# Performance work log

Hardware: AMD Instinct MI355X
Metric: run time of the kernel (lower is better)

Reference implementation:

```python
import jax, jax.numpy as jnp
from jax import lax
import numpy as np

B, T, D, L = 128, 512, 300, 25
H = D // 2  # per-direction LSTM hidden (input_dim // 2)


def setup_inputs() -> dict:
    key = jax.random.key(0)
    ks = jax.random.split(key, 16)
    s = 0.1
    def n(k, shape):
        return jax.random.normal(k, shape, dtype=jnp.float32) * s
    lengths = jax.random.randint(ks[0], (B,), T // 4, T + 1)
    mask = (jnp.arange(T)[None, :] < lengths[:, None]).astype(jnp.float32)
    labels = jax.random.randint(ks[1], (B, T), 0, L)
    return {
        "input_embed": jax.random.normal(ks[2], (B, T, D), dtype=jnp.float32),
        "mask": mask,
        "labels": labels,
        "Wih_f": n(ks[3], (4 * H, D)), "Whh_f": n(ks[4], (4 * H, H)),
        "bih_f": n(ks[5], (4 * H,)), "bhh_f": n(ks[6], (4 * H,)),
        "Wih_b": n(ks[7], (4 * H, D)), "Whh_b": n(ks[8], (4 * H, H)),
        "bih_b": n(ks[9], (4 * H,)), "bhh_b": n(ks[10], (4 * H,)),
        "Wl": n(ks[11], (L, D)), "bl": n(ks[12], (L,)),
        "trans": n(ks[13], (L, L)),
        "start_trans": n(ks[14], (L,)),
        "end_trans": n(ks[15], (L,)),
    }


def _lstm(x, Wih, Whh, bih, bhh):
    # x: (B, T, D) -> hidden states (B, T, H); PyTorch gate order i,f,g,o
    b = bih + bhh
    h0 = jnp.zeros((x.shape[0], H), x.dtype)
    c0 = jnp.zeros((x.shape[0], H), x.dtype)
    def step(carry, xt):
        h, c = carry
        g = xt @ Wih.T + h @ Whh.T + b
        i, f, gg, o = jnp.split(g, 4, axis=-1)
        c = jax.nn.sigmoid(f) * c + jax.nn.sigmoid(i) * jnp.tanh(gg)
        h = jax.nn.sigmoid(o) * jnp.tanh(c)
        return (h, c), h
    _, hs = lax.scan(step, (h0, c0), jnp.swapaxes(x, 0, 1))
    return jnp.swapaxes(hs, 0, 1)


def _emissions(input_embed, mask, Wih_f, Whh_f, bih_f, bhh_f, Wih_b, Whh_b, bih_b, bhh_b, Wl, bl):
    lengths = mask.sum(1).astype(jnp.int32)  # (B,)
    h_f = _lstm(input_embed, Wih_f, Whh_f, bih_f, bhh_f)
    # per-sequence reversal (pack_padded_sequence semantics for the bwd dir)
    idx = jnp.clip(lengths[:, None] - 1 - jnp.arange(T)[None, :], 0, T - 1)  # (B, T)
    idx3 = jnp.broadcast_to(idx[:, :, None], input_embed.shape)
    x_rev = jnp.take_along_axis(input_embed, idx3, axis=1)
    h_b_rev = _lstm(x_rev, Wih_b, Whh_b, bih_b, bhh_b)
    h_b = jnp.take_along_axis(h_b_rev, jnp.broadcast_to(idx[:, :, None], h_b_rev.shape), axis=1)
    # pad_packed_sequence zeros padded positions
    h = jnp.concatenate([h_f, h_b], axis=-1) * mask[:, :, None]
    out = (h @ Wl.T + bl) * mask[:, :, None]  # out *= mask.unsqueeze(-1)
    return out


def _crf_numerator(out, labels, mask, trans, start_trans, end_trans):
    lengths = mask.sum(1).astype(jnp.int32)
    emit = jnp.take_along_axis(out, labels[:, :, None], axis=2)[..., 0]  # (B, T)
    emit_score = jnp.sum(emit * mask, axis=1)
    trans_score = jnp.sum(trans[labels[:, :-1], labels[:, 1:]] * mask[:, 1:], axis=1)
    ar = jnp.arange(out.shape[0])
    y_last = labels[ar, lengths - 1]
    return start_trans[labels[:, 0]] + emit_score + trans_score + end_trans[y_last]


def _crf_denominator(out, mask, trans, start_trans, end_trans):
    alpha0 = start_trans[None, :] + out[:, 0]  # (B, L)
    e_seq = jnp.swapaxes(out, 0, 1)[1:]  # (T-1, B, L)
    m_seq = mask.T[1:]  # (T-1, B)
    def step(alpha, inp):
        e_t, m_t = inp
        new = jax.nn.logsumexp(alpha[:, :, None] + trans[None, :, :], axis=1) + e_t
        alpha = jnp.where((m_t > 0)[:, None], new, alpha)
        return alpha, None
    alpha, _ = lax.scan(step, alpha0, (e_seq, m_seq))
    return jax.nn.logsumexp(alpha + end_trans[None, :], axis=1)


def _viterbi(out, mask, trans, start_trans, end_trans):
    delta0 = start_trans[None, :] + out[:, 0]
    e_seq = jnp.swapaxes(out, 0, 1)[1:]
    m_seq = mask.T[1:]
    ident = jnp.arange(L, dtype=jnp.int32)[None, :]
    def step(delta, inp):
        e_t, m_t = inp
        s = delta[:, :, None] + trans[None, :, :]  # (B, L_prev, L_cur)
        bp = jnp.argmax(s, axis=1).astype(jnp.int32)
        new = jnp.max(s, axis=1) + e_t
        v = (m_t > 0)[:, None]
        return jnp.where(v, new, delta), jnp.where(v, bp, ident)
    delta, bps = lax.scan(step, delta0, (e_seq, m_seq))
    last = jnp.argmax(delta + end_trans[None, :], axis=1).astype(jnp.int32)  # (B,)
    def back(lab, bp):
        prev = jnp.take_along_axis(bp, lab[:, None], axis=1)[:, 0]
        return prev, lab
    lab0, rest = lax.scan(back, last, bps, reverse=True)  # rest[k] = label at t=k+1
    path = jnp.concatenate([lab0[None, :], rest], axis=0)  # (T, B)
    return path.T  # (B, T); positions past each length repeat trailing labels (masked anyway)


def reference(input_embed, mask, labels, Wih_f, Whh_f, bih_f, bhh_f, Wih_b, Whh_b, bih_b, bhh_b, Wl, bl, trans, start_trans, end_trans):
    out = _emissions(input_embed, mask, Wih_f, Whh_f, bih_f, bhh_f, Wih_b, Whh_b, bih_b, bhh_b, Wl, bl)
    score = _crf_numerator(out, labels, mask, trans, start_trans, end_trans) - _crf_denominator(out, mask, trans, start_trans, end_trans)
    loss = -jnp.mean(score)
    path = _viterbi(out, mask, trans, start_trans, end_trans)
    return loss, path
```

## Files before the change

kernel.cpp:

```cpp
#include <hip/hip_runtime.h>
#include <math.h>

#define Bn 128
#define Tn 512
#define Dn 300
#define Hn 150
#define Gn 600
#define Ln 25

__global__ __launch_bounds__(64) void k_len(const float* __restrict__ mask, int* __restrict__ lens) {
  int b = blockIdx.x, lane = threadIdx.x;
  float s = 0.f;
  for (int t = lane; t < Tn; t += 64) s += mask[b * Tn + t];
#pragma unroll
  for (int off = 32; off; off >>= 1) s += __shfl_xor(s, off);
  if (lane == 0) lens[b] = (int)(s + 0.5f);
}

__global__ __launch_bounds__(256) void k_gemm_in(
    const float* __restrict__ X, const float* __restrict__ Wf, const float* __restrict__ Wb,
    const float* __restrict__ bihf, const float* __restrict__ bhhf,
    const float* __restrict__ bihb, const float* __restrict__ bhhb,
    const int* __restrict__ lens, float* __restrict__ XgfC, float* __restrict__ YbC,
    int lo_f, int lo_b, int tshift, int chSh) {
  const int tileR = blockIdx.x;
  const int b = tileR >> tshift;
  const int tloc = (tileR & ((1 << tshift) - 1)) << 6;
  const int dir = (blockIdx.y >= 10);
  const int t_lo = dir ? lo_b : lo_f;
  const int t0g = t_lo + tloc;
  if (t0g >= lens[b]) return;
  const int c0 = (blockIdx.y - dir * 10) << 6;

  __shared__ __align__(16) float As[16][64];
  __shared__ __align__(16) float Bs[16][64];
  const int tid = threadIdx.x;
  const int lr = tid >> 2;
  const int kg = (tid & 3) << 2;
  const int tx = tid & 15, ty = tid >> 4;
  float acc[4][4];
#pragma unroll
  for (int i = 0; i < 4; ++i)
#pragma unroll
    for (int j = 0; j < 4; ++j) acc[i][j] = 0.f;

  const float* Xrow = X + ((size_t)(b * Tn + t0g + lr)) * Dn;
  const int cgl = c0 + lr;
  const float* Wrow = (cgl < Gn) ? ((dir ? Wb : Wf) + (size_t)cgl * Dn) : nullptr;

  for (int k0 = 0; k0 < Dn; k0 += 16) {
    float4 av = make_float4(0.f, 0.f, 0.f, 0.f), bv = make_float4(0.f, 0.f, 0.f, 0.f);
    int k = k0 + kg;
    if (k < Dn) {
      av = *(const float4*)(Xrow + k);
      if (Wrow) bv = *(const float4*)(Wrow + k);
    }
    __syncthreads();
    As[kg + 0][lr] = av.x; As[kg + 1][lr] = av.y; As[kg + 2][lr] = av.z; As[kg + 3][lr] = av.w;
    Bs[kg + 0][lr] = bv.x; Bs[kg + 1][lr] = bv.y; Bs[kg + 2][lr] = bv.z; Bs[kg + 3][lr] = bv.w;
    __syncthreads();
#pragma unroll
    for (int kk = 0; kk < 16; ++kk) {
      float4 a = *(const float4*)(&As[kk][ty << 2]);
      float4 q = *(const float4*)(&Bs[kk][tx << 2]);
      acc[0][0] = fmaf(a.x, q.x, acc[0][0]); acc[0][1] = fmaf(a.x, q.y, acc[0][1]);
      acc[0][2] = fmaf(a.x, q.z, acc[0][2]); acc[0][3] = fmaf(a.x, q.w, acc[0][3]);
      acc[1][0] = fmaf(a.y, q.x, acc[1][0]); acc[1][1] = fmaf(a.y, q.y, acc[1][1]);
      acc[1][2] = fmaf(a.y, q.z, acc[1][2]); acc[1][3] = fmaf(a.y, q.w, acc[1][3]);
      acc[2][0] = fmaf(a.z, q.x, acc[2][0]); acc[2][1] = fmaf(a.z, q.y, acc[2][1]);
      acc[2][2] = fmaf(a.z, q.z, acc[2][2]); acc[2][3] = fmaf(a.z, q.w, acc[2][3]);
      acc[3][0] = fmaf(a.w, q.x, acc[3][0]); acc[3][1] = fmaf(a.w, q.y, acc[3][1]);
      acc[3][2] = fmaf(a.w, q.z, acc[3][2]); acc[3][3] = fmaf(a.w, q.w, acc[3][3]);
    }
  }
  const int cg0 = c0 + (tx << 2);
  if (cg0 >= Gn) return;
  const float* bih = dir ? bihb : bihf;
  const float* bhh = dir ? bhhb : bhhf;
  float* out = dir ? YbC : XgfC;
  const size_t rowbase = ((size_t)b << chSh) + tloc;
#pragma unroll
  for (int i = 0; i < 4; ++i) {
    float4 r;
    r.x = acc[i][0] + bih[cg0 + 0] + bhh[cg0 + 0];
    r.y = acc[i][1] + bih[cg0 + 1] + bhh[cg0 + 1];
    r.z = acc[i][2] + bih[cg0 + 2] + bhh[cg0 + 2];
    r.w = acc[i][3] + bih[cg0 + 3] + bhh[cg0 + 3];
    *(float4*)(out + (rowbase + (ty << 2) + i) * Gn + cg0) = r;
  }
}

__global__ __launch_bounds__(640) void k_lstm(
    const float* __restrict__ XgfC, const float* __restrict__ YbC,
    const float* __restrict__ Whf, const float* __restrict__ Whb,
    const int* __restrict__ lens, float* __restrict__ hf, float* __restrict__ hb,
    float* __restrict__ sHf, float* __restrict__ sCf,
    float* __restrict__ sHb, float* __restrict__ sCb,
    int lo_f, int lo_b, int chSh, int CH) {
  __shared__ __align__(16) float h_s[152];
  __shared__ __align__(16) float g_s[Gn];
  const int tid = threadIdx.x;
  const int dir = blockIdx.x >> 7;
  const int b = blockIdx.x & 127;
  const int len = lens[b];
  const int lo = dir ? lo_b : lo_f;
  if (lo >= len) return;
  const int hi = min(lo + CH, len);
  const float* Xg = dir ? YbC : XgfC;
  const float* W = dir ? Whb : Whf;
  float* ho = dir ? hb : hf;
  float* sH = dir ? sHb : sHf;
  float* sC = dir ? sCb : sCf;
  const bool init = dir ? (hi == len) : (lo == 0);

  if (tid < 152) h_s[tid] = 0.f;
  float c = 0.f;
  if (!init && tid < Hn) { h_s[tid] = sH[b * Hn + tid]; c = sC[b * Hn + tid]; }

  const int col = tid;
  float wreg[152];
  if (col < Gn) {
    const float2* wr = (const float2*)(W + (size_t)col * Hn);
#pragma unroll
    for (int k = 0; k < 75; ++k) {
      float2 w2 = wr[k];
      wreg[2 * k] = w2.x; wreg[2 * k + 1] = w2.y;
    }
    wreg[150] = 0.f; wreg[151] = 0.f;
  } else {
#pragma unroll
    for (int k = 0; k < 152; ++k) wreg[k] = 0.f;
  }
  __syncthreads();

  const int nst = hi - lo;
  const size_t cb = ((size_t)b << chSh);
  const size_t bT = (size_t)b * Tn;
  float xcur = 0.f;
  if (col < Gn) xcur = Xg[(cb + (dir ? (hi - 1 - lo) : 0)) * Gn + col];
  for (int s = 0; s < nst; ++s) {
    const int rl = dir ? (hi - 1 - lo - s) : s;
    const int rg = lo + rl;
    float xn = 0.f;
    if (col < Gn && s + 1 < nst) {
      int rln = dir ? (rl - 1) : (rl + 1);
      xn = Xg[(cb + rln) * Gn + col];
    }
    if (col < Gn) {
      float acc = xcur;
#pragma unroll
      for (int q = 0; q < 38; ++q) {
        float4 h4 = *(const float4*)(h_s + (q << 2));
        acc = fmaf(wreg[q * 4 + 0], h4.x, acc);
        acc = fmaf(wreg[q * 4 + 1], h4.y, acc);
        acc = fmaf(wreg[q * 4 + 2], h4.z, acc);
        acc = fmaf(wreg[q * 4 + 3], h4.w, acc);
      }
      g_s[col] = acc;
    }
    xcur = xn;
    __syncthreads();
    if (tid < Hn) {
      float gi = g_s[tid], gf = g_s[tid + 150], gg = g_s[tid + 300], go = g_s[tid + 450];
      float si = 1.f / (1.f + expf(-gi));
      float sf = 1.f / (1.f + expf(-gf));
      float so = 1.f / (1.f + expf(-go));
      c = sf * c + si * tanhf(gg);
      float h = so * tanhf(c);
      h_s[tid] = h;
      ho[(bT + rg) * Hn + tid] = h;
    }
    __syncthreads();
  }
  if (tid < Hn) { sH[b * Hn + tid] = h_s[tid]; sC[b * Hn + tid] = c; }
}

__global__ __launch_bounds__(256) void k_emis(
    const float* __restrict__ hf, const float* __restrict__ hb,
    const float* __restrict__ Wl, const float* __restrict__ bl,
    const int* __restrict__ lens, float* __restrict__ em) {
  int idx = blockIdx.x * 256 + threadIdx.x;
  int row = idx >> 5;
  int l = idx & 31;
  int b = row >> 9, t = row & 511;
  if (l >= Ln || t >= lens[b]) return;
  const float2* hf2 = (const float2*)(hf + (size_t)row * Hn);
  const float2* hb2 = (const float2*)(hb + (size_t)row * Hn);
  const float2* w0 = (const float2*)(Wl + (size_t)l * Dn);
  const float2* w1 = (const float2*)(Wl + (size_t)l * Dn + Hn);
  float acc = bl[l];
#pragma unroll 5
  for (int q = 0; q < 75; ++q) {
    float2 a = hf2[q], w = w0[q];
    acc = fmaf(a.x, w.x, fmaf(a.y, w.y, acc));
    float2 a2 = hb2[q], w2 = w1[q];
    acc = fmaf(a2.x, w2.x, fmaf(a2.y, w2.y, acc));
  }
  em[(size_t)row * Ln + l] = acc;
}

__global__ __launch_bounds__(64) void k_num(
    const float* __restrict__ em, const int* __restrict__ labels, const int* __restrict__ lens,
    const float* __restrict__ trans, const float* __restrict__ st, const float* __restrict__ et,
    float* __restrict__ num) {
  int b = blockIdx.x, lane = threadIdx.x;
  int len = lens[b];
  float s = 0.f;
  for (int t = lane; t < len; t += 64) {
    int lab = labels[b * Tn + t];
    s += em[((size_t)b * Tn + t) * Ln + lab];
    if (t + 1 < len) s += trans[lab * Ln + labels[b * Tn + t + 1]];
  }
#pragma unroll
  for (int off = 32; off; off >>= 1) s += __shfl_xor(s, off);
  if (lane == 0)
    num[b] = s + st[labels[b * Tn]] + et[labels[b * Tn + len - 1]];
}

__global__ __launch_bounds__(64) void k_den(
    const float* __restrict__ em, const int* __restrict__ lens, const float* __restrict__ trans,
    const float* __restrict__ st, const float* __restrict__ et, float* __restrict__ den) {
  __shared__ float E[Ln * Ln];
  __shared__ float p_s[32];
  int b = blockIdx.x, lane = threadIdx.x;
  for (int u = lane; u < Ln * Ln; u += 64) E[u] = expf(trans[u]);
  int len = lens[b];
  const float* ob = em + (size_t)b * Tn * Ln;
  float alpha = -1e30f;
  if (lane < Ln) alpha = st[lane] + ob[lane];
  __syncthreads();
  for (int t = 1; t < len; ++t) {
    float m = alpha;
#pragma unroll
    for (int off = 32; off; off >>= 1) m = fmaxf(m, __shfl_xor(m, off));
    float p = (lane < Ln) ? expf(alpha - m) : 0.f;
    if (lane < 32) p_s[lane] = p;
    __syncthreads();
    if (lane < Ln) {
      float ssum = 0.f;
#pragma unroll
      for (int i = 0; i < Ln; ++i) ssum = fmaf(p_s[i], E[i * Ln + lane], ssum);
      alpha = m + logf(ssum) + ob[(size_t)t * Ln + lane];
    }
    __syncthreads();
  }
  float v = (lane < Ln) ? alpha + et[lane] : -1e30f;
  float m = v;
#pragma unroll
  for (int off = 32; off; off >>= 1) m = fmaxf(m, __shfl_xor(m, off));
  float ex = (lane < Ln) ? expf(v - m) : 0.f;
#pragma unroll
  for (int off = 32; off; off >>= 1) ex += __shfl_xor(ex, off);
  if (lane == 0) den[b] = m + logf(ex);
}

__global__ __launch_bounds__(64) void k_vit(
    const float* __restrict__ em, const int* __restrict__ lens, const float* __restrict__ trans,
    const float* __restrict__ st, const float* __restrict__ et, float* __restrict__ pathf) {
  __shared__ float Tl[Ln * Ln];
  __shared__ float d_s[Ln];
  __shared__ unsigned char bp[Tn * Ln];
  int b = blockIdx.x, lane = threadIdx.x;
  for (int u = lane; u < Ln * Ln; u += 64) Tl[u] = trans[u];
  int len = lens[b];
  const float* ob = em + (size_t)b * Tn * Ln;
  float delta = (lane < Ln) ? st[lane] + ob[lane] : -1e30f;
  __syncthreads();
  for (int t = 1; t < len; ++t) {
    if (lane < Ln) d_s[lane] = delta;
    __syncthreads();
    if (lane < Ln) {
      float best = -1e30f; int bi = 0;
#pragma unroll
      for (int i = 0; i < Ln; ++i) {
        float v = d_s[i] + Tl[i * Ln + lane];
        if (v > best) { best = v; bi = i; }
      }
      bp[t * Ln + lane] = (unsigned char)bi;
      delta = best + ob[(size_t)t * Ln + lane];
    }
    __syncthreads();
  }
  float v = (lane < Ln) ? delta + et[lane] : -1e30f;
  float m = v;
#pragma unroll
  for (int off = 32; off; off >>= 1) m = fmaxf(m, __shfl_xor(m, off));
  unsigned long long eq = __ballot(v == m);
  int last = __ffsll(eq) - 1;
  if (lane == 0) {
    int cur = last;
    for (int t = len - 1; t >= 1; --t) {
      pathf[b * Tn + t] = (float)cur;
      cur = bp[t * Ln + cur];
    }
    pathf[b * Tn + 0] = (float)cur;
  }
  for (int t = len + lane; t < Tn; t += 64)
    pathf[b * Tn + t] = (float)last;
}

__global__ __launch_bounds__(64) void k_loss(const float* __restrict__ num, const float* __restrict__ den,
                                             float* __restrict__ out0) {
  int lane = threadIdx.x;
  float s = (num[lane] - den[lane]) + (num[lane + 64] - den[lane + 64]);
#pragma unroll
  for (int off = 32; off; off >>= 1) s += __shfl_xor(s, off);
  if (lane == 0) out0[0] = -s / (float)Bn;
}

extern "C" void kernel_launch(void* const* d_in, const int* in_sizes, int n_in,
                              void* d_out, int out_size, void* d_ws, size_t ws_size,
                              hipStream_t stream) {
  const float* X = (const float*)d_in[0];
  const float* mask = (const float*)d_in[1];
  const int* labels = (const int*)d_in[2];
  const float* Wihf = (const float*)d_in[3];
  const float* Whhf = (const float*)d_in[4];
  const float* bihf = (const float*)d_in[5];
  const float* bhhf = (const float*)d_in[6];
  const float* Wihb = (const float*)d_in[7];
  const float* Whhb = (const float*)d_in[8];
  const float* bihb = (const float*)d_in[9];
  const float* bhhb = (const float*)d_in[10];
  const float* Wl = (const float*)d_in[11];
  const float* bl = (const float*)d_in[12];
  const float* trans = (const float*)d_in[13];
  const float* st = (const float*)d_in[14];
  const float* et = (const float*)d_in[15];
  float* outv = (float*)d_out;

  auto planBytes = [](int CH) -> size_t {
    return ((size_t)2 * Bn * CH * Gn + 2 * (size_t)Bn * Tn * Hn + (size_t)Bn * Tn * Ln
            + 4 * (size_t)Bn * Hn + 3 * (size_t)Bn) * 4;
  };
  int CH, chSh, tshift;
  if (ws_size >= planBytes(512)) { CH = 512; chSh = 9; tshift = 3; }
  else                           { CH = 64;  chSh = 6; tshift = 0; }
  const int NC = Tn / CH;

  float* ws = (float*)d_ws;
  size_t off = 0;
  float* XgfC = ws + off; off += (size_t)Bn * CH * Gn;
  float* YbC  = ws + off; off += (size_t)Bn * CH * Gn;
  float* hf   = ws + off; off += (size_t)Bn * Tn * Hn;
  float* hb   = ws + off; off += (size_t)Bn * Tn * Hn;
  float* em   = ws + off; off += (size_t)Bn * Tn * Ln;
  float* sHf  = ws + off; off += (size_t)Bn * Hn;
  float* sCf  = ws + off; off += (size_t)Bn * Hn;
  float* sHb  = ws + off; off += (size_t)Bn * Hn;
  float* sCb  = ws + off; off += (size_t)Bn * Hn;
  float* num  = ws + off; off += Bn;
  float* den  = ws + off; off += Bn;
  int* lens   = (int*)(ws + off); off += Bn;

  k_len<<<Bn, 64, 0, stream>>>(mask, lens);

  for (int i = 0; i < NC; ++i) {
    int lo_f = i * CH;
    int lo_b = (NC - 1 - i) * CH;
    dim3 gg(Bn * (CH >> 6), 20);
    k_gemm_in<<<gg, 256, 0, stream>>>(X, Wihf, Wihb, bihf, bhhf, bihb, bhhb,
                                      lens, XgfC, YbC, lo_f, lo_b, tshift, chSh);
    k_lstm<<<2 * Bn, 640, 0, stream>>>(XgfC, YbC, Whhf, Whhb, lens, hf, hb,
                                       sHf, sCf, sHb, sCb, lo_f, lo_b, chSh, CH);
  }

  k_emis<<<(Bn * Tn * 32) / 256, 256, 0, stream>>>(hf, hb, Wl, bl, lens, em);

  k_num<<<Bn, 64, 0, stream>>>(em, labels, lens, trans, st, et, num);
  k_den<<<Bn, 64, 0, stream>>>(em, lens, trans, st, et, den);
  k_vit<<<Bn, 64, 0, stream>>>(em, lens, trans, st, et, outv + 1);
  k_loss<<<1, 64, 0, stream>>>(num, den, outv);
}
```

Before: 2.572 ms.

## Fuse CRF kernels into one launch, double-buffer input GEMM, add chunk sizes

Merges the numerator, forward-algorithm and Viterbi kernels into a single 384-block launch in which each block takes one role. The denominator and Viterbi roles stage emissions in shared memory and hold a transition column in registers, using wave shuffles in place of per-step shared-memory exchanges and barriers. The input-projection GEMM gains a double-buffered shared tile with the next global load issued before compute, dropping one barrier per k-step. Intermediate chunk sizes are added for mid-sized workspaces. The costs are higher register and shared-memory use (about 64KB per CRF block) and possibly lower occupancy.

After: 2.136 ms. -17.0%, faster.

```diff
diff --git a/kernel.cpp b/kernel.cpp
--- a/kernel.cpp
+++ b/kernel.cpp
@@ -32,8 +32,8 @@
   if (t0g >= lens[b]) return;
   const int c0 = (blockIdx.y - dir * 10) << 6;
 
-  __shared__ __align__(16) float As[16][64];
-  __shared__ __align__(16) float Bs[16][64];
+  __shared__ __align__(16) float As[2][16][64];
+  __shared__ __align__(16) float Bs[2][16][64];
   const int tid = threadIdx.x;
   const int lr = tid >> 2;
   const int kg = (tid & 3) << 2;
@@ -48,21 +48,29 @@
   const int cgl = c0 + lr;
   const float* Wrow = (cgl < Gn) ? ((dir ? Wb : Wf) + (size_t)cgl * Dn) : nullptr;
 
+  float4 av = make_float4(0.f, 0.f, 0.f, 0.f), bv = make_float4(0.f, 0.f, 0.f, 0.f);
+  {
+    int k = kg;
+    av = *(const float4*)(Xrow + k);
+    if (Wrow) bv = *(const float4*)(Wrow + k);
+  }
+  int buf = 0;
   for (int k0 = 0; k0 < Dn; k0 += 16) {
-    float4 av = make_float4(0.f, 0.f, 0.f, 0.f), bv = make_float4(0.f, 0.f, 0.f, 0.f);
-    int k = k0 + kg;
-    if (k < Dn) {
-      av = *(const float4*)(Xrow + k);
-      if (Wrow) bv = *(const float4*)(Wrow + k);
-    }
+    As[buf][kg + 0][lr] = av.x; As[buf][kg + 1][lr] = av.y;
+    As[buf][kg + 2][lr] = av.z; As[buf][kg + 3][lr] = av.w;
+    Bs[buf][kg + 0][lr] = bv.x; Bs[buf][kg + 1][lr] = bv.y;
+    Bs[buf][kg + 2][lr] = bv.z; Bs[buf][kg + 3][lr] = bv.w;
     __syncthreads();
-    As[kg + 0][lr] = av.x; As[kg + 1][lr] = av.y; As[kg + 2][lr] = av.z; As[kg + 3][lr] = av.w;
-    Bs[kg + 0][lr] = bv.x; Bs[kg + 1][lr] = bv.y; Bs[kg + 2][lr] = bv.z; Bs[kg + 3][lr] = bv.w;
-    __syncthreads();
+    av = make_float4(0.f, 0.f, 0.f, 0.f); bv = make_float4(0.f, 0.f, 0.f, 0.f);
+    int kn = k0 + 16 + kg;
+    if (kn < Dn) {
+      av = *(const float4*)(Xrow + kn);
+      if (Wrow) bv = *(const float4*)(Wrow + kn);
+    }
 #pragma unroll
     for (int kk = 0; kk < 16; ++kk) {
-      float4 a = *(const float4*)(&As[kk][ty << 2]);
-      float4 q = *(const float4*)(&Bs[kk][tx << 2]);
+      float4 a = *(const float4*)(&As[buf][kk][ty << 2]);
+      float4 q = *(const float4*)(&Bs[buf][kk][tx << 2]);
       acc[0][0] = fmaf(a.x, q.x, acc[0][0]); acc[0][1] = fmaf(a.x, q.y, acc[0][1]);
       acc[0][2] = fmaf(a.x, q.z, acc[0][2]); acc[0][3] = fmaf(a.x, q.w, acc[0][3]);
       acc[1][0] = fmaf(a.y, q.x, acc[1][0]); acc[1][1] = fmaf(a.y, q.y, acc[1][1]);
@@ -72,6 +80,7 @@
       acc[3][0] = fmaf(a.w, q.x, acc[3][0]); acc[3][1] = fmaf(a.w, q.y, acc[3][1]);
       acc[3][2] = fmaf(a.w, q.z, acc[3][2]); acc[3][3] = fmaf(a.w, q.w, acc[3][3]);
     }
+    buf ^= 1;
   }
   const int cg0 = c0 + (tx << 2);
   if (cg0 >= Gn) return;
@@ -199,87 +208,84 @@
   em[(size_t)row * Ln + l] = acc;
 }
 
-__global__ __launch_bounds__(64) void k_num(
+__global__ __launch_bounds__(64) void k_crf(
     const float* __restrict__ em, const int* __restrict__ labels, const int* __restrict__ lens,
     const float* __restrict__ trans, const float* __restrict__ st, const float* __restrict__ et,
-    float* __restrict__ num) {
-  int b = blockIdx.x, lane = threadIdx.x;
-  int len = lens[b];
-  float s = 0.f;
-  for (int t = lane; t < len; t += 64) {
-    int lab = labels[b * Tn + t];
-    s += em[((size_t)b * Tn + t) * Ln + lab];
-    if (t + 1 < len) s += trans[lab * Ln + labels[b * Tn + t + 1]];
-  }
-#pragma unroll
-  for (int off = 32; off; off >>= 1) s += __shfl_xor(s, off);
-  if (lane == 0)
-    num[b] = s + st[labels[b * Tn]] + et[labels[b * Tn + len - 1]];
-}
-
-__global__ __launch_bounds__(64) void k_den(
-    const float* __restrict__ em, const int* __restrict__ lens, const float* __restrict__ trans,
-    const float* __restrict__ st, const float* __restrict__ et, float* __restrict__ den) {
-  __shared__ float E[Ln * Ln];
-  __shared__ float p_s[32];
-  int b = blockIdx.x, lane = threadIdx.x;
-  for (int u = lane; u < Ln * Ln; u += 64) E[u] = expf(trans[u]);
-  int len = lens[b];
+    float* __restrict__ den, float* __restrict__ num, float* __restrict__ pathf) {
+  const int role = blockIdx.x >> 7;
+  const int b = blockIdx.x & 127;
+  const int lane = threadIdx.x;
+  const int len = lens[b];
+
+  if (role == 2) {
+    float s = 0.f;
+    for (int t = lane; t < len; t += 64) {
+      int lab = labels[b * Tn + t];
+      s += em[((size_t)b * Tn + t) * Ln + lab];
+      if (t + 1 < len) s += trans[lab * Ln + labels[b * Tn + t + 1]];
+    }
+#pragma unroll
+    for (int off = 32; off; off >>= 1) s += __shfl_xor(s, off);
+    if (lane == 0)
+      num[b] = s + st[labels[b * Tn]] + et[labels[b * Tn + len - 1]];
+    return;
+  }
+
+  __shared__ __align__(16) float em_s[Tn * Ln];
+  __shared__ unsigned char bp[Tn * Ln];
+
   const float* ob = em + (size_t)b * Tn * Ln;
-  float alpha = -1e30f;
-  if (lane < Ln) alpha = st[lane] + ob[lane];
+  {
+    const float4* ob4 = (const float4*)ob;
+    float4* es4 = (float4*)em_s;
+    int n4 = (len * Ln + 3) >> 2;
+    for (int u = lane; u < n4; u += 64) es4[u] = ob4[u];
+  }
+  const int cl = (lane < Ln) ? lane : 0;
+  float col[Ln];
+  if (role == 0) {
+#pragma unroll
+    for (int i = 0; i < Ln; ++i) col[i] = expf(trans[i * Ln + cl]);
+  } else {
+#pragma unroll
+    for (int i = 0; i < Ln; ++i) col[i] = trans[i * Ln + cl];
+  }
   __syncthreads();
+
+  if (role == 0) {
+    float alpha = (lane < Ln) ? st[lane] + em_s[lane] : -1e30f;
+    for (int t = 1; t < len; ++t) {
+      float m = alpha;
+#pragma unroll
+      for (int off = 32; off; off >>= 1) m = fmaxf(m, __shfl_xor(m, off));
+      float p = (lane < Ln) ? expf(alpha - m) : 0.f;
+      float ssum = 0.f;
+#pragma unroll
+      for (int i = 0; i < Ln; ++i) ssum = fmaf(__shfl(p, i), col[i], ssum);
+      float e_t = em_s[t * Ln + cl];
+      alpha = (lane < Ln) ? m + logf(ssum) + e_t : -1e30f;
+    }
+    float v = (lane < Ln) ? alpha + et[lane] : -1e30f;
+    float m = v;
+#pragma unroll
+    for (int off = 32; off; off >>= 1) m = fmaxf(m, __shfl_xor(m, off));
+    float ex = (lane < Ln) ? expf(v - m) : 0.f;
+#pragma unroll
+    for (int off = 32; off; off >>= 1) ex += __shfl_xor(ex, off);
+    if (lane == 0) den[b] = m + logf(ex);
+    return;
+  }
+
+  float delta = (lane < Ln) ? st[lane] + em_s[lane] : -1e30f;
   for (int t = 1; t < len; ++t) {
-    float m = alpha;
-#pragma unroll
-    for (int off = 32; off; off >>= 1) m = fmaxf(m, __shfl_xor(m, off));
-    float p = (lane < Ln) ? expf(alpha - m) : 0.f;
-    if (lane < 32) p_s[lane] = p;
-    __syncthreads();
-    if (lane < Ln) {
-      float ssum = 0.f;
-#pragma unroll
-      for (int i = 0; i < Ln; ++i) ssum = fmaf(p_s[i], E[i * Ln + lane], ssum);
-      alpha = m + logf(ssum) + ob[(size_t)t * Ln + lane];
-    }
-    __syncthreads();
-  }
-  float v = (lane < Ln) ? alpha + et[lane] : -1e30f;
-  float m = v;
-#pragma unroll
-  for (int off = 32; off; off >>= 1) m = fmaxf(m, __shfl_xor(m, off));
-  float ex = (lane < Ln) ? expf(v - m) : 0.f;
-#pragma unroll
-  for (int off = 32; off; off >>= 1) ex += __shfl_xor(ex, off);
-  if (lane == 0) den[b] = m + logf(ex);
-}
-
-__global__ __launch_bounds__(64) void k_vit(
-    const float* __restrict__ em, const int* __restrict__ lens, const float* __restrict__ trans,
-    const float* __restrict__ st, const float* __restrict__ et, float* __restrict__ pathf) {
-  __shared__ float Tl[Ln * Ln];
-  __shared__ float d_s[Ln];
-  __shared__ unsigned char bp[Tn * Ln];
-  int b = blockIdx.x, lane = threadIdx.x;
-  for (int u = lane; u < Ln * Ln; u += 64) Tl[u] = trans[u];
-  int len = lens[b];
-  const float* ob = em + (size_t)b * Tn * Ln;
-  float delta = (lane < Ln) ? st[lane] + ob[lane] : -1e30f;
-  __syncthreads();
-  for (int t = 1; t < len; ++t) {
-    if (lane < Ln) d_s[lane] = delta;
-    __syncthreads();
-    if (lane < Ln) {
-      float best = -1e30f; int bi = 0;
-#pragma unroll
-      for (int i = 0; i < Ln; ++i) {
-        float v = d_s[i] + Tl[i * Ln + lane];
-        if (v > best) { best = v; bi = i; }
-      }
-      bp[t * Ln + lane] = (unsigned char)bi;
-      delta = best + ob[(size_t)t * Ln + lane];
-    }
-    __syncthreads();
+    float best = -1e30f; int bi = 0;
+#pragma unroll
+    for (int i = 0; i < Ln; ++i) {
+      float v = __shfl(delta, i) + col[i];
+      if (v > best) { best = v; bi = i; }
+    }
+    if (lane < Ln) bp[t * Ln + lane] = (unsigned char)bi;
+    delta = (lane < Ln) ? best + em_s[t * Ln + cl] : -1e30f;
   }
   float v = (lane < Ln) ? delta + et[lane] : -1e30f;
   float m = v;
@@ -287,6 +293,7 @@
   for (int off = 32; off; off >>= 1) m = fmaxf(m, __shfl_xor(m, off));
   unsigned long long eq = __ballot(v == m);
   int last = __ffsll(eq) - 1;
+  __syncthreads();
   if (lane == 0) {
     int cur = last;
     for (int t = len - 1; t >= 1; --t) {
@@ -333,9 +340,12 @@
     return ((size_t)2 * Bn * CH * Gn + 2 * (size_t)Bn * Tn * Hn + (size_t)Bn * Tn * Ln
             + 4 * (size_t)Bn * Hn + 3 * (size_t)Bn) * 4;
   };
-  int CH, chSh, tshift;
-  if (ws_size >= planBytes(512)) { CH = 512; chSh = 9; tshift = 3; }
-  else                           { CH = 64;  chSh = 6; tshift = 0; }
+  int CH, chSh;
+  if      (ws_size >= planBytes(512)) { CH = 512; chSh = 9; }
+  else if (ws_size >= planBytes(256)) { CH = 256; chSh = 8; }
+  else if (ws_size >= planBytes(128)) { CH = 128; chSh = 7; }
+  else                                { CH = 64;  chSh = 6; }
+  const int tshift = chSh - 6;
   const int NC = Tn / CH;
 
   float* ws = (float*)d_ws;
@@ -367,8 +377,6 @@
 
   k_emis<<<(Bn * Tn * 32) / 256, 256, 0, stream>>>(hf, hb, Wl, bl, lens, em);
 
-  k_num<<<Bn, 64, 0, stream>>>(em, labels, lens, trans, st, et, num);
-  k_den<<<Bn, 64, 0, stream>>>(em, lens, trans, st, et, den);
-  k_vit<<<Bn, 64, 0, stream>>>(em, lens, trans, st, et, outv + 1);
+  k_crf<<<384, 64, 0, stream>>>(em, labels, lens, trans, st, et, den, num, outv + 1);
   k_loss<<<1, 64, 0, stream>>>(num, den, outv);
 }
```
